# Optimization experiments

Hardware: AMD Instinct MI355X
Metric: run time of the kernel (lower is better)

## Reference

```python
import jax, jax.numpy as jnp
import numpy as np

N_HEAD = 16
N_FEAT = 1024
D_K = N_FEAT // N_HEAD


def rtt_half(x):
    x1, x2 = x[..., : x.shape[-1] // 2], x[..., x.shape[-1] // 2 :]
    return jnp.concatenate([-x2, x1], axis=-1)


def setup_inputs() -> dict:
    key = jax.random.key(0)
    ks = jax.random.split(key, 16)
    B, T, D = 4, 2048, N_FEAT
    inp = {
        "query": jax.random.normal(ks[0], (B, T, D), jnp.float32),
        "key": jax.random.normal(ks[1], (B, T, D), jnp.float32),
        "value": jax.random.normal(ks[2], (B, T, D), jnp.float32),
        "cos": jax.random.uniform(ks[3], (T, 1, D_K), jnp.float32),
        "sin": jax.random.uniform(ks[4], (T, 1, D_K), jnp.float32),
        "mask": jnp.zeros((B, T, T), jnp.bool_),
    }
    s = 1.0 / np.sqrt(D)
    inp["Wq"] = jax.random.uniform(ks[5], (D, D), jnp.float32, -s, s)
    inp["bq"] = jax.random.uniform(ks[6], (D,), jnp.float32, -s, s)
    inp["Wk"] = jax.random.uniform(ks[7], (D, D), jnp.float32, -s, s)
    inp["bk"] = jax.random.uniform(ks[8], (D,), jnp.float32, -s, s)
    inp["Wv"] = jax.random.uniform(ks[9], (D, D), jnp.float32, -s, s)
    inp["bv"] = jax.random.uniform(ks[10], (D,), jnp.float32, -s, s)
    inp["Wo"] = jax.random.uniform(ks[11], (D, D), jnp.float32, -s, s)
    inp["bo"] = jax.random.uniform(ks[12], (D,), jnp.float32, -s, s)
    return inp


def reference(query, key, value, cos, sin, mask, Wq, bq, Wk, bk, Wv, bv, Wo, bo):
    B, T, D = query.shape
    h, d_k = N_HEAD, D_K
    # QKV projections (torch Linear: x @ W.T + b), reshape to (B,T,h,d_k)
    q = (query @ Wq.T + bq).reshape(B, T, h, d_k)
    k = (key @ Wk.T + bk).reshape(B, T, h, d_k)
    v = (value @ Wv.T + bv).reshape(B, T, h, d_k)
    # RoPE: cos/sin sliced to T, broadcast (T,1,d_k) over (B,T,h,d_k)
    c, s = cos[:T], sin[:T]
    q = q * c + rtt_half(q) * s
    k = k * c + rtt_half(k) * s
    # attention scores (B,h,T,T)
    scores = jnp.einsum("bqhd,bkhd->bhqk", q, k) / np.sqrt(d_k).astype(jnp.float32)
    scores = jnp.where(mask[:, None, :, :], -jnp.inf, scores)
    attn = jax.nn.softmax(scores, axis=-1)
    out = jnp.einsum("bhqk,bkhd->bqhd", attn, v).reshape(B, T, D)
    return out @ Wo.T + bo
```

## Files before the change

### kernel.cpp

```cpp
#include <hip/hip_runtime.h>

#define B_SZ 4
#define T_SZ 2048
#define D_SZ 1024
#define H_SZ 16
#define DK_SZ 64
#define M_SZ (B_SZ * T_SZ)

typedef __attribute__((ext_vector_type(8))) short bf16x8;
typedef __attribute__((ext_vector_type(4))) short bf16x4;
typedef __attribute__((ext_vector_type(4))) float f32x4;

union fui { float f; unsigned u; };

static __device__ inline short f2bf(float x) {
    union { float f; unsigned u; } v; v.f = x;
    unsigned r = v.u + 0x7fff + ((v.u >> 16) & 1);
    return (short)(r >> 16);
}
static __device__ inline void split1(float f, short* h, short* l) {
    fui a; a.f = f;
    *h = (short)(a.u >> 16);
    fui t; t.u = a.u & 0xffff0000u;
    fui r; r.f = f - t.f;
    *l = (short)(r.u >> 16);
}

#define MFMA16(a, b, c) __builtin_amdgcn_mfma_f32_16x16x32_bf16((a), (b), (c), 0, 0, 0)

#define GLDS16(g, l) __builtin_amdgcn_global_load_lds(                        \
    (const __attribute__((address_space(1))) unsigned int*)(g),               \
    (__attribute__((address_space(3))) unsigned int*)(l), 16, 0, 0)

__global__ __launch_bounds__(256)
void wsplit_kernel(const float* __restrict__ W, short* __restrict__ Wh,
                   short* __restrict__ Wl)
{
    const int i = blockIdx.x * 256 + threadIdx.x;
    float4 f = ((const float4*)W)[i];
    fui a[4]; a[0].f = f.x; a[1].f = f.y; a[2].f = f.z; a[3].f = f.w;
    union { short s[4]; short4 v; } H, L;
#pragma unroll
    for (int j = 0; j < 4; ++j) {
        H.s[j] = (short)(a[j].u >> 16);
        fui t; t.u = a[j].u & 0xffff0000u;
        fui r; r.f = a[j].f - t.f;
        L.s[j] = (short)(r.u >> 16);
    }
    ((short4*)Wh)[i] = H.v;
    ((short4*)Wl)[i] = L.v;
}

__global__ __launch_bounds__(256)
void mask_flags_kernel(const unsigned char* __restrict__ mask, int* __restrict__ flags)
{
    const int f = blockIdx.x * 4 + (threadIdx.x >> 6);
    const int lane = threadIdx.x & 63;
    const int b = f >> 10, qt = (f >> 5) & 31, kt = f & 31;
    const unsigned char* base = mask + ((size_t)b * T_SZ + qt * 64) * T_SZ + kt * 64;
    bool nz = false;
#pragma unroll
    for (int i = 0; i < 4; ++i) {
        const int c = lane + 64 * i;
        const int row = c >> 2, off = (c & 3) * 16;
        uint4 v = *(const uint4*)(base + (size_t)row * T_SZ + off);
        nz |= ((v.x | v.y | v.z | v.w) != 0);
    }
    unsigned long long bal = __ballot(nz);
    if (lane == 0) flags[f] = (bal != 0) ? 1 : 0;
}

__global__ __launch_bounds__(256)
void qkv_mfma_kernel(const short* __restrict__ Ah, const short* __restrict__ Al,
                     const short* __restrict__ Wh, const short* __restrict__ Wl,
                     const float* __restrict__ bias,
                     const float* __restrict__ cosb, const float* __restrict__ sinb,
                     short* __restrict__ Hd, short* __restrict__ Ld,
                     short* __restrict__ Vb, const int which)
{
    __shared__ __align__(16) short Ahs[128 * 32];
    __shared__ __align__(16) short Als[128 * 32];
    __shared__ __align__(16) short Whs[128 * 32];
    __shared__ __align__(16) short Wls[128 * 32];

    const int m0 = blockIdx.x * 128, n0 = blockIdx.y * 128;
    const int tid = threadIdx.x;
    const int wv = tid >> 6, lane = tid & 63;
    const int wm = wv >> 1, wn = wv & 1;
    const int l15 = lane & 15, quad = lane >> 4;

    f32x4 acc[4][4];
#pragma unroll
    for (int mt = 0; mt < 4; ++mt)
#pragma unroll
        for (int nt = 0; nt < 4; ++nt)
            acc[mt][nt] = (f32x4){0.f, 0.f, 0.f, 0.f};

    const size_t aoff = (size_t)(m0 + wv * 32 + (lane >> 2)) * D_SZ + (lane & 3) * 8;
    const size_t woff = (size_t)(n0 + wv * 32 + (lane >> 2)) * D_SZ + (lane & 3) * 8;
    const short* ahg = Ah + aoff;
    const short* alg = Al + aoff;
    const short* whg = Wh + woff;
    const short* wlg = Wl + woff;
    short* ah0 = &Ahs[wv * 1024];
    short* al0 = &Als[wv * 1024];
    short* wh0 = &Whs[wv * 1024];
    short* wl0 = &Wls[wv * 1024];

    for (int k0 = 0; k0 < D_SZ; k0 += 32) {
        __syncthreads();
        GLDS16(ahg + k0,             ah0);
        GLDS16(ahg + 16 * D_SZ + k0, ah0 + 512);
        GLDS16(alg + k0,             al0);
        GLDS16(alg + 16 * D_SZ + k0, al0 + 512);
        GLDS16(whg + k0,             wh0);
        GLDS16(whg + 16 * D_SZ + k0, wh0 + 512);
        GLDS16(wlg + k0,             wl0);
        GLDS16(wlg + 16 * D_SZ + k0, wl0 + 512);
        __syncthreads();

        bf16x8 ah[4], al[4];
#pragma unroll
        for (int mt = 0; mt < 4; ++mt) {
            const int arow = (wm * 64 + mt * 16 + l15) * 32 + quad * 8;
            ah[mt] = *(const bf16x8*)&Ahs[arow];
            al[mt] = *(const bf16x8*)&Als[arow];
        }
#pragma unroll
        for (int nt = 0; nt < 4; ++nt) {
            const int brow = (wn * 64 + nt * 16 + l15) * 32 + quad * 8;
            const bf16x8 bh = *(const bf16x8*)&Whs[brow];
            const bf16x8 bl = *(const bf16x8*)&Wls[brow];
#pragma unroll
            for (int mt = 0; mt < 4; ++mt) {
                acc[mt][nt] = MFMA16(ah[mt], bh, acc[mt][nt]);
                acc[mt][nt] = MFMA16(al[mt], bh, acc[mt][nt]);
                acc[mt][nt] = MFMA16(ah[mt], bl, acc[mt][nt]);
            }
        }
    }

    const int hh = (blockIdx.y << 1) + wn;
    if (which < 2) {
        const float qscale = (which == 0) ? 0.125f : 1.0f;
#pragma unroll
        for (int mt = 0; mt < 4; ++mt)
#pragma unroll
            for (int p = 0; p < 2; ++p) {
                const int d1 = p * 16 + l15, d2 = d1 + 32;
                const int col1 = n0 + wn * 64 + d1;
                const float b1 = bias[col1], b2 = bias[col1 + 32];
#pragma unroll
                for (int r = 0; r < 4; ++r) {
                    const int m = m0 + wm * 64 + mt * 16 + quad * 4 + r;
                    const int bb = m >> 11, tg = m & (T_SZ - 1);
                    const float c1 = cosb[tg * 64 + d1], s1 = sinb[tg * 64 + d1];
                    const float c2 = cosb[tg * 64 + d2], s2 = sinb[tg * 64 + d2];
                    const float x1 = acc[mt][p][r] + b1;
                    const float x2 = acc[mt][p + 2][r] + b2;
                    const float y1 = (x1 * c1 - x2 * s1) * qscale;
                    const float y2 = (x2 * c2 + x1 * s2) * qscale;
                    const size_t base = (((size_t)(bb * H_SZ + hh)) * T_SZ + tg) * 64;
                    short h_, l_;
                    split1(y1, &h_, &l_); Hd[base + d1] = h_; Ld[base + d1] = l_;
                    split1(y2, &h_, &l_); Hd[base + d2] = h_; Ld[base + d2] = l_;
                }
            }
    } else {
#pragma unroll
        for (int nt = 0; nt < 4; ++nt) {
            const int d = nt * 16 + l15;
            const float bvv = bias[n0 + wn * 64 + d];
#pragma unroll
            for (int mt = 0; mt < 4; ++mt)
#pragma unroll
                for (int r = 0; r < 4; ++r) {
                    const int m = m0 + wm * 64 + mt * 16 + quad * 4 + r;
                    const int bb = m >> 11, tg = m & (T_SZ - 1);
                    Vb[(((size_t)(bb * H_SZ + hh)) * T_SZ + tg) * 64 + d] =
                        f2bf(acc[mt][nt][r] + bvv);
                }
        }
    }
}

__global__ __launch_bounds__(256)
void gemm_out_kernel(const short* __restrict__ Ah, const short* __restrict__ Al,
                     const short* __restrict__ Wh, const short* __restrict__ Wl,
                     const float* __restrict__ bias, float* __restrict__ C)
{
    __shared__ __align__(16) short Ahs[128 * 32];
    __shared__ __align__(16) short Als[128 * 32];
    __shared__ __align__(16) short Whs[128 * 32];
    __shared__ __align__(16) short Wls[128 * 32];

    const int m0 = blockIdx.x * 128, n0 = blockIdx.y * 128;
    const int tid = threadIdx.x;
    const int wv = tid >> 6, lane = tid & 63;
    const int wm = wv >> 1, wn = wv & 1;
    const int l15 = lane & 15, quad = lane >> 4;

    f32x4 acc[4][4];
#pragma unroll
    for (int mt = 0; mt < 4; ++mt)
#pragma unroll
        for (int nt = 0; nt < 4; ++nt)
            acc[mt][nt] = (f32x4){0.f, 0.f, 0.f, 0.f};

    const size_t aoff = (size_t)(m0 + wv * 32 + (lane >> 2)) * D_SZ + (lane & 3) * 8;
    const size_t woff = (size_t)(n0 + wv * 32 + (lane >> 2)) * D_SZ + (lane & 3) * 8;
    const short* ahg = Ah + aoff;
    const short* alg = Al + aoff;
    const short* whg = Wh + woff;
    const short* wlg = Wl + woff;
    short* ah0 = &Ahs[wv * 1024];
    short* al0 = &Als[wv * 1024];
    short* wh0 = &Whs[wv * 1024];
    short* wl0 = &Wls[wv * 1024];

    for (int k0 = 0; k0 < D_SZ; k0 += 32) {
        __syncthreads();
        GLDS16(ahg + k0,             ah0);
        GLDS16(ahg + 16 * D_SZ + k0, ah0 + 512);
        GLDS16(alg + k0,             al0);
        GLDS16(alg + 16 * D_SZ + k0, al0 + 512);
        GLDS16(whg + k0,             wh0);
        GLDS16(whg + 16 * D_SZ + k0, wh0 + 512);
        GLDS16(wlg + k0,             wl0);
        GLDS16(wlg + 16 * D_SZ + k0, wl0 + 512);
        __syncthreads();

        bf16x8 ah[4], al[4];
#pragma unroll
        for (int mt = 0; mt < 4; ++mt) {
            const int arow = (wm * 64 + mt * 16 + l15) * 32 + quad * 8;
            ah[mt] = *(const bf16x8*)&Ahs[arow];
            al[mt] = *(const bf16x8*)&Als[arow];
        }
#pragma unroll
        for (int nt = 0; nt < 4; ++nt) {
            const int brow = (wn * 64 + nt * 16 + l15) * 32 + quad * 8;
            const bf16x8 bh = *(const bf16x8*)&Whs[brow];
            const bf16x8 bl = *(const bf16x8*)&Wls[brow];
#pragma unroll
            for (int mt = 0; mt < 4; ++mt) {
                acc[mt][nt] = MFMA16(ah[mt], bh, acc[mt][nt]);
                acc[mt][nt] = MFMA16(al[mt], bh, acc[mt][nt]);
                acc[mt][nt] = MFMA16(ah[mt], bl, acc[mt][nt]);
            }
        }
    }

#pragma unroll
    for (int nt = 0; nt < 4; ++nt) {
        const int col = n0 + wn * 64 + nt * 16 + l15;
        const float bvv = bias[col];
#pragma unroll
        for (int mt = 0; mt < 4; ++mt)
#pragma unroll
            for (int r = 0; r < 4; ++r) {
                const int m = m0 + wm * 64 + mt * 16 + quad * 4 + r;
                C[(size_t)m * D_SZ + col] = acc[mt][nt][r] + bvv;
            }
    }
}

__global__ __launch_bounds__(256)
void attn_mfma_kernel(const short* __restrict__ Qhg, const short* __restrict__ Qlg,
                      const short* __restrict__ Khg, const short* __restrict__ Klg,
                      const short* __restrict__ Vg,
                      const unsigned char* __restrict__ mask,
                      const int* __restrict__ flags,
                      short* __restrict__ Oh, short* __restrict__ Ol)
{
    __shared__ __align__(16) short Khs[64 * 72];
    __shared__ __align__(16) short Kls[64 * 72];
    __shared__ __align__(16) short Vt[64 * 72];
    __shared__ __align__(16) short Ps[4 * 16 * 72];

    const int bh = blockIdx.y;
    const int b = bh >> 4, h = bh & 15;
    const int q0 = blockIdx.x * 64;
    const int tid = threadIdx.x;
    const int wv = tid >> 6, lane = tid & 63;
    const int l15 = lane & 15, quad = lane >> 4;

    const short* qhp = Qhg + ((size_t)bh * T_SZ + q0 + wv * 16 + l15) * 64 + quad * 8;
    const short* qlp = Qlg + ((size_t)bh * T_SZ + q0 + wv * 16 + l15) * 64 + quad * 8;
    bf16x8 qh[2], ql[2];
#pragma unroll
    for (int s = 0; s < 2; ++s) {
        qh[s] = *(const bf16x8*)(qhp + 32 * s);
        ql[s] = *(const bf16x8*)(qlp + 32 * s);
    }

    f32x4 accO[4];
#pragma unroll
    for (int nt = 0; nt < 4; ++nt) accO[nt] = (f32x4){0.f, 0.f, 0.f, 0.f};
    float m_i[4], l_i[4];
#pragma unroll
    for (int r = 0; r < 4; ++r) { m_i[r] = -1e30f; l_i[r] = 0.f; }

    const short* khb = Khg + (size_t)bh * T_SZ * 64;
    const short* klb = Klg + (size_t)bh * T_SZ * 64;
    const short* vb  = Vg  + (size_t)bh * T_SZ * 64;
    const unsigned char* mbase = mask + ((size_t)b * T_SZ + q0) * T_SZ;
    const int* frow = flags + ((size_t)b * 32 + blockIdx.x) * 32;

    const short* kgp[4];
    short*       kld[4];
#pragma unroll
    for (int jj = 0; jj < 4; ++jj) {
        const int cc = tid + 256 * (jj & 1);
        const int row = cc >> 3, off = (cc & 7) * 8;
        kgp[jj] = ((jj < 2) ? khb : klb) + (size_t)row * 64 + off;
        kld[jj] = ((jj < 2) ? Khs : Kls) + row * 72 + off;
    }
    const int vt0 = (tid & 15) * 4, vd0 = (tid >> 4) * 4;
    const short* vgp[4];
#pragma unroll
    for (int i = 0; i < 4; ++i)
        vgp[i] = vb + (size_t)(vt0 + i) * 64 + vd0;
    short* pw = &Ps[wv * 16 * 72];

    bf16x8 kst[4];
    uint2  rv[4];
#pragma unroll
    for (int jj = 0; jj < 4; ++jj) kst[jj] = *(const bf16x8*)(kgp[jj]);
#pragma unroll
    for (int i = 0; i < 4; ++i)    rv[i]   = *(const uint2*)(vgp[i]);

    for (int kti = 0; kti < 32; ++kti) {
        const int kt = kti * 64;
        __syncthreads();
#pragma unroll
        for (int jj = 0; jj < 4; ++jj)
            *(bf16x8*)kld[jj] = kst[jj];
#pragma unroll
        for (int c = 0; c < 4; ++c) {
            const int k = c >> 1;
            const unsigned sel = (c & 1) ? 0x07060302u : 0x05040100u;
            const unsigned lo0 = k ? rv[0].y : rv[0].x;
            const unsigned lo1 = k ? rv[1].y : rv[1].x;
            const unsigned lo2 = k ? rv[2].y : rv[2].x;
            const unsigned lo3 = k ? rv[3].y : rv[3].x;
            uint2 o;
            o.x = __builtin_amdgcn_perm(lo1, lo0, sel);
            o.y = __builtin_amdgcn_perm(lo3, lo2, sel);
            *(uint2*)&Vt[(vd0 + c) * 72 + vt0] = o;
        }
        if (kti < 31) {
            const size_t adv = (size_t)(kt + 64) * 64;
#pragma unroll
            for (int jj = 0; jj < 4; ++jj)
                kst[jj] = *(const bf16x8*)(kgp[jj] + adv);
#pragma unroll
            for (int i = 0; i < 4; ++i)
                rv[i] = *(const uint2*)(vgp[i] + adv);
        }
        __syncthreads();

        f32x4 accS[4];
        __builtin_amdgcn_s_setprio(1);
#pragma unroll
        for (int nt = 0; nt < 4; ++nt) {
            f32x4 acc = (f32x4){0.f, 0.f, 0.f, 0.f};
#pragma unroll
            for (int s = 0; s < 2; ++s) {
                const bf16x8 kh = *(const bf16x8*)&Khs[(nt * 16 + l15) * 72 + 32 * s + quad * 8];
                const bf16x8 kl = *(const bf16x8*)&Kls[(nt * 16 + l15) * 72 + 32 * s + quad * 8];
                acc = MFMA16(qh[s], kh, acc);
                acc = MFMA16(ql[s], kh, acc);
                acc = MFMA16(qh[s], kl, acc);
            }
            accS[nt] = acc;
        }
        __builtin_amdgcn_s_setprio(0);

        float sv[4][4];
        if (frow[kti]) {
#pragma unroll
            for (int nt = 0; nt < 4; ++nt)
#pragma unroll
                for (int r = 0; r < 4; ++r) {
                    const unsigned char mb =
                        mbase[(size_t)(wv * 16 + quad * 4 + r) * T_SZ + kt + nt * 16 + l15];
                    sv[nt][r] = mb ? -1e30f : accS[nt][r];
                }
        } else {
#pragma unroll
            for (int nt = 0; nt < 4; ++nt)
#pragma unroll
                for (int r = 0; r < 4; ++r)
                    sv[nt][r] = accS[nt][r];
        }

        float rmax[4];
#pragma unroll
        for (int r = 0; r < 4; ++r)
            rmax[r] = fmaxf(fmaxf(sv[0][r], sv[1][r]), fmaxf(sv[2][r], sv[3][r]));
#pragma unroll
        for (int off = 1; off < 16; off <<= 1)
#pragma unroll
            for (int r = 0; r < 4; ++r)
                rmax[r] = fmaxf(rmax[r], __shfl_xor(rmax[r], off, 64));

        float alpha[4];
#pragma unroll
        for (int r = 0; r < 4; ++r) {
            const float mnew = fmaxf(m_i[r], rmax[r]);
            alpha[r] = __expf(m_i[r] - mnew);
            m_i[r] = mnew;
        }
        float lsum[4] = {0.f, 0.f, 0.f, 0.f};
#pragma unroll
        for (int nt = 0; nt < 4; ++nt)
#pragma unroll
            for (int r = 0; r < 4; ++r) {
                const float p = __expf(sv[nt][r] - m_i[r]);
                sv[nt][r] = p;
                lsum[r] += p;
            }
#pragma unroll
        for (int r = 0; r < 4; ++r)
            l_i[r] = l_i[r] * alpha[r] + lsum[r];

#pragma unroll
        for (int nt = 0; nt < 4; ++nt)
#pragma unroll
            for (int r = 0; r < 4; ++r) {
                fui u; u.f = sv[nt][r];
                pw[(quad * 4 + r) * 72 + nt * 16 + l15] = (short)((u.u + 0x8000u) >> 16);
            }

#pragma unroll
        for (int nt = 0; nt < 4; ++nt)
#pragma unroll
            for (int r = 0; r < 4; ++r)
                accO[nt][r] *= alpha[r];

        bf16x8 pa[2];
#pragma unroll
        for (int s = 0; s < 2; ++s)
            pa[s] = *(const bf16x8*)&pw[l15 * 72 + 32 * s + quad * 8];
        __builtin_amdgcn_s_setprio(1);
#pragma unroll
        for (int nt = 0; nt < 4; ++nt)
#pragma unroll
            for (int s = 0; s < 2; ++s) {
                const bf16x8 vf = *(const bf16x8*)&Vt[(nt * 16 + l15) * 72 + 32 * s + quad * 8];
                accO[nt] = MFMA16(pa[s], vf, accO[nt]);
            }
        __builtin_amdgcn_s_setprio(0);
    }

#pragma unroll
    for (int off = 1; off < 16; off <<= 1)
#pragma unroll
        for (int r = 0; r < 4; ++r)
            l_i[r] += __shfl_xor(l_i[r], off, 64);

#pragma unroll
    for (int r = 0; r < 4; ++r) {
        const float inv = 1.f / l_i[r];
        const int t = q0 + wv * 16 + quad * 4 + r;
        const size_t base = ((size_t)(b * T_SZ + t)) * D_SZ + h * DK_SZ;
#pragma unroll
        for (int nt = 0; nt < 4; ++nt) {
            short h_, l_;
            split1(accO[nt][r] * inv, &h_, &l_);
            Oh[base + nt * 16 + l15] = h_;
            Ol[base + nt * 16 + l15] = l_;
        }
    }
}

extern "C" void kernel_launch(void* const* d_in, const int* in_sizes, int n_in,
                              void* d_out, int out_size, void* d_ws, size_t ws_size,
                              hipStream_t stream)
{
    const float* query = (const float*)d_in[0];
    const float* key   = (const float*)d_in[1];
    const float* value = (const float*)d_in[2];
    const float* cosb  = (const float*)d_in[3];
    const float* sinb  = (const float*)d_in[4];
    const unsigned char* mask = (const unsigned char*)d_in[5];
    const float* Wq = (const float*)d_in[6];
    const float* bq = (const float*)d_in[7];
    const float* Wk = (const float*)d_in[8];
    const float* bk = (const float*)d_in[9];
    const float* Wv = (const float*)d_in[10];
    const float* bv = (const float*)d_in[11];
    const float* Wo = (const float*)d_in[12];
    const float* bo = (const float*)d_in[13];
    float* out = (float*)d_out;

    short* sp = (short*)d_ws;
    const size_t eb = (size_t)B_SZ * H_SZ * T_SZ * DK_SZ;
    short* Qh = sp;          short* Ql = sp + eb;
    short* Kh = sp + 2 * eb; short* Kl = sp + 3 * eb;
    short* Vb = sp + 4 * eb;
    short* Xh = sp + 5 * eb; short* Xl = sp + 6 * eb;
    short* wsp = sp + 7 * eb;
    const size_t wlen = (size_t)D_SZ * D_SZ;
    short* wqh = wsp;            short* wql = wsp + wlen;
    short* wkh = wsp + 2 * wlen; short* wkl = wsp + 3 * wlen;
    short* wvh = wsp + 4 * wlen; short* wvl = wsp + 5 * wlen;
    short* woh = wsp + 6 * wlen; short* wol = wsp + 7 * wlen;
    int* flags = (int*)(wsp + 8 * wlen);

    const int wsBlocks = (int)(wlen / 4 / 256);
    const int aBlocks  = (int)((size_t)M_SZ * D_SZ / 4 / 256);
    wsplit_kernel<<<wsBlocks, 256, 0, stream>>>(Wq, wqh, wql);
    wsplit_kernel<<<wsBlocks, 256, 0, stream>>>(Wk, wkh, wkl);
    wsplit_kernel<<<wsBlocks, 256, 0, stream>>>(Wv, wvh, wvl);
    wsplit_kernel<<<wsBlocks, 256, 0, stream>>>(Wo, woh, wol);

    mask_flags_kernel<<<1024, 256, 0, stream>>>(mask, flags);

    wsplit_kernel<<<aBlocks, 256, 0, stream>>>(query, Xh, Xl);
    qkv_mfma_kernel<<<dim3(M_SZ / 128, 8), 256, 0, stream>>>(
        Xh, Xl, wqh, wql, bq, cosb, sinb, Qh, Ql, Vb, 0);
    wsplit_kernel<<<aBlocks, 256, 0, stream>>>(key, Xh, Xl);
    qkv_mfma_kernel<<<dim3(M_SZ / 128, 8), 256, 0, stream>>>(
        Xh, Xl, wkh, wkl, bk, cosb, sinb, Kh, Kl, Vb, 1);
    wsplit_kernel<<<aBlocks, 256, 0, stream>>>(value, Xh, Xl);
    qkv_mfma_kernel<<<dim3(M_SZ / 128, 8), 256, 0, stream>>>(
        Xh, Xl, wvh, wvl, bv, cosb, sinb, Qh, Ql, Vb, 2);

    attn_mfma_kernel<<<dim3(T_SZ / 64, B_SZ * H_SZ), 256, 0, stream>>>(
        Qh, Ql, Kh, Kl, Vb, mask, flags, Xh, Xl);

    gemm_out_kernel<<<dim3(M_SZ / 128, D_SZ / 128), 256, 0, stream>>>(
        Xh, Xl, woh, wol, bo, out);
}
```

Measured before the change: 665.5 us.

## Double-buffer GEMM LDS staging, use exp2 with lazy softmax rescale, swizzle attention blocks

```diff
diff --git a/kernel.cpp b/kernel.cpp
--- a/kernel.cpp
+++ b/kernel.cpp
@@ -8,7 +8,6 @@
 #define M_SZ (B_SZ * T_SZ)
 
 typedef __attribute__((ext_vector_type(8))) short bf16x8;
-typedef __attribute__((ext_vector_type(4))) short bf16x4;
 typedef __attribute__((ext_vector_type(4))) float f32x4;
 
 union fui { float f; unsigned u; };
@@ -78,10 +77,10 @@
                      short* __restrict__ Hd, short* __restrict__ Ld,
                      short* __restrict__ Vb, const int which)
 {
-    __shared__ __align__(16) short Ahs[128 * 32];
-    __shared__ __align__(16) short Als[128 * 32];
-    __shared__ __align__(16) short Whs[128 * 32];
-    __shared__ __align__(16) short Wls[128 * 32];
+    __shared__ __align__(16) short Ahs[2][4096];
+    __shared__ __align__(16) short Als[2][4096];
+    __shared__ __align__(16) short Whs[2][4096];
+    __shared__ __align__(16) short Wls[2][4096];
 
     const int m0 = blockIdx.x * 128, n0 = blockIdx.y * 128;
     const int tid = threadIdx.x;
@@ -102,35 +101,41 @@
     const short* alg = Al + aoff;
     const short* whg = Wh + woff;
     const short* wlg = Wl + woff;
-    short* ah0 = &Ahs[wv * 1024];
-    short* al0 = &Als[wv * 1024];
-    short* wh0 = &Whs[wv * 1024];
-    short* wl0 = &Wls[wv * 1024];
-
+
+#define STAGEQ(bi, kk)                                                        \
+    do {                                                                      \
+        short* a0 = &Ahs[bi][wv * 1024];                                      \
+        short* a1 = &Als[bi][wv * 1024];                                      \
+        short* w0 = &Whs[bi][wv * 1024];                                      \
+        short* w1 = &Wls[bi][wv * 1024];                                      \
+        GLDS16(ahg + (kk),             a0);                                   \
+        GLDS16(ahg + 16 * D_SZ + (kk), a0 + 512);                             \
+        GLDS16(alg + (kk),             a1);                                   \
+        GLDS16(alg + 16 * D_SZ + (kk), a1 + 512);                             \
+        GLDS16(whg + (kk),             w0);                                   \
+        GLDS16(whg + 16 * D_SZ + (kk), w0 + 512);                             \
+        GLDS16(wlg + (kk),             w1);                                   \
+        GLDS16(wlg + 16 * D_SZ + (kk), w1 + 512);                             \
+    } while (0)
+
+    STAGEQ(0, 0);
     for (int k0 = 0; k0 < D_SZ; k0 += 32) {
+        const int cur = (k0 >> 5) & 1;
         __syncthreads();
-        GLDS16(ahg + k0,             ah0);
-        GLDS16(ahg + 16 * D_SZ + k0, ah0 + 512);
-        GLDS16(alg + k0,             al0);
-        GLDS16(alg + 16 * D_SZ + k0, al0 + 512);
-        GLDS16(whg + k0,             wh0);
-        GLDS16(whg + 16 * D_SZ + k0, wh0 + 512);
-        GLDS16(wlg + k0,             wl0);
-        GLDS16(wlg + 16 * D_SZ + k0, wl0 + 512);
-        __syncthreads();
+        if (k0 + 32 < D_SZ) STAGEQ(cur ^ 1, k0 + 32);
 
         bf16x8 ah[4], al[4];
 #pragma unroll
         for (int mt = 0; mt < 4; ++mt) {
             const int arow = (wm * 64 + mt * 16 + l15) * 32 + quad * 8;
-            ah[mt] = *(const bf16x8*)&Ahs[arow];
-            al[mt] = *(const bf16x8*)&Als[arow];
+            ah[mt] = *(const bf16x8*)&Ahs[cur][arow];
+            al[mt] = *(const bf16x8*)&Als[cur][arow];
         }
 #pragma unroll
         for (int nt = 0; nt < 4; ++nt) {
             const int brow = (wn * 64 + nt * 16 + l15) * 32 + quad * 8;
-            const bf16x8 bh = *(const bf16x8*)&Whs[brow];
-            const bf16x8 bl = *(const bf16x8*)&Wls[brow];
+            const bf16x8 bh = *(const bf16x8*)&Whs[cur][brow];
+            const bf16x8 bl = *(const bf16x8*)&Wls[cur][brow];
 #pragma unroll
             for (int mt = 0; mt < 4; ++mt) {
                 acc[mt][nt] = MFMA16(ah[mt], bh, acc[mt][nt]);
@@ -139,10 +144,11 @@
             }
         }
     }
+#undef STAGEQ
 
     const int hh = (blockIdx.y << 1) + wn;
     if (which < 2) {
-        const float qscale = (which == 0) ? 0.125f : 1.0f;
+        const float qscale = (which == 0) ? 0.125f * 1.4426950408889634f : 1.0f;
 #pragma unroll
         for (int mt = 0; mt < 4; ++mt)
 #pragma unroll
@@ -189,10 +195,10 @@
                      const short* __restrict__ Wh, const short* __restrict__ Wl,
                      const float* __restrict__ bias, float* __restrict__ C)
 {
-    __shared__ __align__(16) short Ahs[128 * 32];
-    __shared__ __align__(16) short Als[128 * 32];
-    __shared__ __align__(16) short Whs[128 * 32];
-    __shared__ __align__(16) short Wls[128 * 32];
+    __shared__ __align__(16) short Ahs[2][4096];
+    __shared__ __align__(16) short Als[2][4096];
+    __shared__ __align__(16) short Whs[2][4096];
+    __shared__ __align__(16) short Wls[2][4096];
 
     const int m0 = blockIdx.x * 128, n0 = blockIdx.y * 128;
     const int tid = threadIdx.x;
@@ -213,35 +219,41 @@
     const short* alg = Al + aoff;
     const short* whg = Wh + woff;
     const short* wlg = Wl + woff;
-    short* ah0 = &Ahs[wv * 1024];
-    short* al0 = &Als[wv * 1024];
-    short* wh0 = &Whs[wv * 1024];
-    short* wl0 = &Wls[wv * 1024];
-
+
+#define STAGEO(bi, kk)                                                        \
+    do {                                                                      \
+        short* a0 = &Ahs[bi][wv * 1024];                                      \
+        short* a1 = &Als[bi][wv * 1024];                                      \
+        short* w0 = &Whs[bi][wv * 1024];                                      \
+        short* w1 = &Wls[bi][wv * 1024];                                      \
+        GLDS16(ahg + (kk),             a0);                                   \
+        GLDS16(ahg + 16 * D_SZ + (kk), a0 + 512);                             \
+        GLDS16(alg + (kk),             a1);                                   \
+        GLDS16(alg + 16 * D_SZ + (kk), a1 + 512);                             \
+        GLDS16(whg + (kk),             w0);                                   \
+        GLDS16(whg + 16 * D_SZ + (kk), w0 + 512);                             \
+        GLDS16(wlg + (kk),             w1);                                   \
+        GLDS16(wlg + 16 * D_SZ + (kk), w1 + 512);                             \
+    } while (0)
+
+    STAGEO(0, 0);
     for (int k0 = 0; k0 < D_SZ; k0 += 32) {
+        const int cur = (k0 >> 5) & 1;
         __syncthreads();
-        GLDS16(ahg + k0,             ah0);
-        GLDS16(ahg + 16 * D_SZ + k0, ah0 + 512);
-        GLDS16(alg + k0,             al0);
-        GLDS16(alg + 16 * D_SZ + k0, al0 + 512);
-        GLDS16(whg + k0,             wh0);
-        GLDS16(whg + 16 * D_SZ + k0, wh0 + 512);
-        GLDS16(wlg + k0,             wl0);
-        GLDS16(wlg + 16 * D_SZ + k0, wl0 + 512);
-        __syncthreads();
+        if (k0 + 32 < D_SZ) STAGEO(cur ^ 1, k0 + 32);
 
         bf16x8 ah[4], al[4];
 #pragma unroll
         for (int mt = 0; mt < 4; ++mt) {
             const int arow = (wm * 64 + mt * 16 + l15) * 32 + quad * 8;
-            ah[mt] = *(const bf16x8*)&Ahs[arow];
-            al[mt] = *(const bf16x8*)&Als[arow];
+            ah[mt] = *(const bf16x8*)&Ahs[cur][arow];
+            al[mt] = *(const bf16x8*)&Als[cur][arow];
         }
 #pragma unroll
         for (int nt = 0; nt < 4; ++nt) {
             const int brow = (wn * 64 + nt * 16 + l15) * 32 + quad * 8;
-            const bf16x8 bh = *(const bf16x8*)&Whs[brow];
-            const bf16x8 bl = *(const bf16x8*)&Wls[brow];
+            const bf16x8 bh = *(const bf16x8*)&Whs[cur][brow];
+            const bf16x8 bl = *(const bf16x8*)&Wls[cur][brow];
 #pragma unroll
             for (int mt = 0; mt < 4; ++mt) {
                 acc[mt][nt] = MFMA16(ah[mt], bh, acc[mt][nt]);
@@ -250,6 +262,7 @@
             }
         }
     }
+#undef STAGEO
 
 #pragma unroll
     for (int nt = 0; nt < 4; ++nt) {
@@ -278,9 +291,12 @@
     __shared__ __align__(16) short Vt[64 * 72];
     __shared__ __align__(16) short Ps[4 * 16 * 72];
 
-    const int bh = blockIdx.y;
+    const int lid = blockIdx.y * 32 + blockIdx.x;
+    const int sw  = (lid & 7) * 256 + (lid >> 3);
+    const int bh  = sw >> 5;
+    const int qb  = sw & 31;
     const int b = bh >> 4, h = bh & 15;
-    const int q0 = blockIdx.x * 64;
+    const int q0 = qb * 64;
     const int tid = threadIdx.x;
     const int wv = tid >> 6, lane = tid & 63;
     const int l15 = lane & 15, quad = lane >> 4;
@@ -305,7 +321,7 @@
     const short* klb = Klg + (size_t)bh * T_SZ * 64;
     const short* vb  = Vg  + (size_t)bh * T_SZ * 64;
     const unsigned char* mbase = mask + ((size_t)b * T_SZ + q0) * T_SZ;
-    const int* frow = flags + ((size_t)b * 32 + blockIdx.x) * 32;
+    const int* frow = flags + ((size_t)b * 32 + qb) * 32;
 
     const short* kgp[4];
     short*       kld[4];
@@ -405,25 +421,35 @@
             for (int r = 0; r < 4; ++r)
                 rmax[r] = fmaxf(rmax[r], __shfl_xor(rmax[r], off, 64));
 
-        float alpha[4];
-#pragma unroll
-        for (int r = 0; r < 4; ++r) {
-            const float mnew = fmaxf(m_i[r], rmax[r]);
-            alpha[r] = __expf(m_i[r] - mnew);
-            m_i[r] = mnew;
-        }
+        bool need = false;
+#pragma unroll
+        for (int r = 0; r < 4; ++r)
+            need |= (rmax[r] > m_i[r] + 10.0f);
+        if (__any((int)need)) {
+#pragma unroll
+            for (int r = 0; r < 4; ++r) {
+                const float mnew = fmaxf(m_i[r], rmax[r]);
+                const float alpha = __builtin_exp2f(m_i[r] - mnew);
+                m_i[r] = mnew;
+                l_i[r] *= alpha;
+#pragma unroll
+                for (int nt = 0; nt < 4; ++nt)
+                    accO[nt][r] *= alpha;
+            }
+        }
+
         float lsum[4] = {0.f, 0.f, 0.f, 0.f};
 #pragma unroll
         for (int nt = 0; nt < 4; ++nt)
 #pragma unroll
             for (int r = 0; r < 4; ++r) {
-                const float p = __expf(sv[nt][r] - m_i[r]);
+                const float p = __builtin_exp2f(sv[nt][r] - m_i[r]);
                 sv[nt][r] = p;
                 lsum[r] += p;
             }
 #pragma unroll
         for (int r = 0; r < 4; ++r)
-            l_i[r] = l_i[r] * alpha[r] + lsum[r];
+            l_i[r] += lsum[r];
 
 #pragma unroll
         for (int nt = 0; nt < 4; ++nt)
@@ -432,12 +458,6 @@
                 fui u; u.f = sv[nt][r];
                 pw[(quad * 4 + r) * 72 + nt * 16 + l15] = (short)((u.u + 0x8000u) >> 16);
             }
-
-#pragma unroll
-        for (int nt = 0; nt < 4; ++nt)
-#pragma unroll
-            for (int r = 0; r < 4; ++r)
-                accO[nt][r] *= alpha[r];
 
         bf16x8 pa[2];
 #pragma unroll
```

After: 695.5 us. +4.5%, slower.
